# Performance work log

Measured on AMD Instinct MI355X. Metric: run time of the kernel, lower is better.

## Reference

```python
import jax, jax.numpy as jnp
import numpy as np

N_NODES = 50000
N_EDGES = 800000
K_HOPS = 3


def _gcn_norm(edge_index, num_nodes):
    # PyG gcn_norm with add_self_loops=False: sym normalization by target-degree
    row, col = edge_index[0], edge_index[1]  # source j -> target i
    ones = jnp.ones((edge_index.shape[1],), dtype=jnp.float32)
    deg = jax.ops.segment_sum(ones, col, num_segments=num_nodes)
    dinv = jnp.where(deg > 0, 1.0 / jnp.sqrt(deg), 0.0)
    return dinv[row] * dinv[col]  # [E]


def _propagate(h, row, col, norm, num_nodes):
    # out_i = sum_{j->i} norm_e * h_j   (scatter-add over edges)
    msg = h[row] * norm[:, None]  # [E, d]
    return jax.ops.segment_sum(msg, col, num_segments=num_nodes)


def _tag_conv(x, W, b, row, col, norm, num_nodes):
    # out = sum_{k=0..K} (A_norm^k x) @ W[k] + b
    out = x @ W[0]
    h = x
    for k in range(1, K_HOPS + 1):
        h = _propagate(h, row, col, norm, num_nodes)
        out = out + h @ W[k]
    return out + b


def setup_inputs() -> dict:
    key = jax.random.key(0)
    ks = jax.random.split(key, 12)
    x = jax.random.normal(ks[0], (N_NODES, 16), dtype=jnp.float32)
    edge_index = jax.random.randint(ks[1], (2, N_EDGES), 0, N_NODES, dtype=jnp.int64)
    dims = [(16, 64), (64, 64), (64, 64), (64, 64), (64, 4)]
    inp = {"x": x, "edge_index": edge_index}
    for i, (din, dout) in enumerate(dims):
        scale = 1.0 / np.sqrt(din)
        inp[f"W{i}"] = jax.random.normal(ks[2 + 2 * i], (K_HOPS + 1, din, dout), dtype=jnp.float32) * scale
        inp[f"b{i}"] = jnp.zeros((dout,), dtype=jnp.float32)
    return inp


def reference(x, edge_index, W0, b0, W1, b1, W2, b2, W3, b3, W4, b4):
    num_nodes = x.shape[0]
    row, col = edge_index[0], edge_index[1]
    norm = _gcn_norm(edge_index, num_nodes)
    Ws = [W0, W1, W2, W3, W4]
    bs = [b0, b1, b2, b3, b4]
    h = x
    for i in range(4):  # first len(convs)-1 layers: conv -> dropout(identity, eval) -> relu
        h = _tag_conv(h, Ws[i], bs[i], row, col, norm, num_nodes)
        h = jax.nn.relu(h)
    return _tag_conv(h, Ws[4], bs[4], row, col, norm, num_nodes)
```

## Files before the change

### kernel.cpp

```cpp
#include <hip/hip_runtime.h>
#include <hip/hip_fp16.h>

typedef _Float16 f16x8 __attribute__((ext_vector_type(8)));
typedef float f32x4 __attribute__((ext_vector_type(4)));

union H2I { int i; __half2 h; };
static __device__ inline float2 i2f2(int v) {
    H2I u; u.i = v; return __half22float2(u.h);
}
static __device__ inline int f2i2(float a, float b) {
    H2I u; u.h = __floats2half2_rn(a, b); return u.i;
}

struct F8 { float2 a, b, c, d; };
static __device__ inline void fma8(F8& s, int4 g, float w) {
    float2 t;
    t = i2f2(g.x); s.a.x += w * t.x; s.a.y += w * t.y;
    t = i2f2(g.y); s.b.x += w * t.x; s.b.y += w * t.y;
    t = i2f2(g.z); s.c.x += w * t.x; s.c.y += w * t.y;
    t = i2f2(g.w); s.d.x += w * t.x; s.d.y += w * t.y;
}


__global__ __launch_bounds__(256) void count_rank_kernel(const int* __restrict__ col,
                                                         int* __restrict__ cnt,
                                                         int* __restrict__ rank, int E) {
    int e = blockIdx.x * 256 + threadIdx.x;
    if (e < E) rank[e] = atomicAdd(&cnt[col[e]], 1);
}

__global__ __launch_bounds__(256) void scan_block_kernel(const int* __restrict__ cnt,
                                                         int* __restrict__ off,
                                                         int* __restrict__ bsum, int n) {
    const int gid = blockIdx.x * 256 + threadIdx.x;
    const int v = (gid < n) ? cnt[gid] : 0;
    const int lane = threadIdx.x & 63, w = threadIdx.x >> 6;
    int x = v;
#pragma unroll
    for (int d = 1; d < 64; d <<= 1) {
        int t = __shfl_up(x, d);
        if (lane >= d) x += t;
    }
    __shared__ int wt[4];
    if (lane == 63) wt[w] = x;
    __syncthreads();
    int base = 0;
#pragma unroll
    for (int i = 0; i < 3; ++i)
        if (i < w) base += wt[i];
    const int incl = base + x;
    if (gid < n) off[gid] = incl - v;
    if (threadIdx.x == 255) bsum[blockIdx.x] = incl;
}

__global__ __launch_bounds__(256) void scan_bsum_kernel(const int* __restrict__ bsum,
                                                        int* __restrict__ bbase, int nb) {
    const int tid = threadIdx.x;
    const int v = (tid < nb) ? bsum[tid] : 0;
    const int lane = tid & 63, w = tid >> 6;
    int x = v;
#pragma unroll
    for (int d = 1; d < 64; d <<= 1) {
        int t = __shfl_up(x, d);
        if (lane >= d) x += t;
    }
    __shared__ int wt[4];
    if (lane == 63) wt[w] = x;
    __syncthreads();
    int base = 0;
#pragma unroll
    for (int i = 0; i < 3; ++i)
        if (i < w) base += wt[i];
    if (tid < nb) bbase[tid] = base + x - v;
}

__global__ __launch_bounds__(256) void scan_apply_kernel(int* __restrict__ off,
                                                         const int* __restrict__ bbase,
                                                         int n, int E) {
    const int gid = blockIdx.x * 256 + threadIdx.x;
    if (gid < n) off[gid] += bbase[blockIdx.x];
    if (gid == n) off[n] = E;
}

__global__ __launch_bounds__(256) void dinv_kernel(const int* __restrict__ cnt,
                                                   float* __restrict__ dinv, int n) {
    int i = blockIdx.x * 256 + threadIdx.x;
    if (i < n) {
        int c = cnt[i];
        dinv[i] = (c > 0) ? 1.0f / sqrtf((float)c) : 0.0f;
    }
}

__global__ __launch_bounds__(256) void scatter_kernel(const int* __restrict__ row,
                                                      const int* __restrict__ col,
                                                      const int* __restrict__ off,
                                                      const int* __restrict__ rank,
                                                      const float* __restrict__ dinv,
                                                      int2* __restrict__ recs, int E) {
    int e = blockIdx.x * 256 + threadIdx.x;
    if (e >= E) return;
    const int r = row[e], c = col[e];
    const int pos = off[c] + rank[e];
    recs[pos] = make_int2(r, __float_as_int(dinv[r] * dinv[c]));
}

__global__ __launch_bounds__(256) void tohalf_kernel(const float* __restrict__ in,
                                                     __half* __restrict__ xcat, int N) {
    int i = blockIdx.x * 256 + threadIdx.x;
    if (i >= N * 2) return;
    const int n = i >> 1, q = i & 1;
    const float4 v0 = ((const float4*)in)[n * 4 + q * 2 + 0];
    const float4 v1 = ((const float4*)in)[n * 4 + q * 2 + 1];
    int4 o;
    o.x = f2i2(v0.x, v0.y);
    o.y = f2i2(v0.z, v0.w);
    o.z = f2i2(v1.x, v1.y);
    o.w = f2i2(v1.z, v1.w);
    ((int4*)xcat)[n * 8 + q] = o;
}


template <int DQ, int S4>
__global__ __launch_bounds__(256) void gatherh_kernel(const int* __restrict__ off,
                                                      const int2* __restrict__ recs,
                                                      const __half* __restrict__ hin,
                                                      __half* __restrict__ hout, int nNodes) {
    const int t = blockIdx.x * 256 + threadIdx.x;
    const int n = t / DQ;
    const int q = t & (DQ - 1);
    if (n >= nNodes) return;
    const int4* __restrict__ h4 = (const int4*)hin;
    F8 s = {};
    int e = off[n];
    const int e1 = off[n + 1];
    for (; e + 4 <= e1; e += 4) {
        const int2 r0 = recs[e + 0];
        const int2 r1 = recs[e + 1];
        const int2 r2 = recs[e + 2];
        const int2 r3 = recs[e + 3];
        const int4 g0 = h4[r0.x * S4 + q];
        const int4 g1 = h4[r1.x * S4 + q];
        const int4 g2 = h4[r2.x * S4 + q];
        const int4 g3 = h4[r3.x * S4 + q];
        fma8(s, g0, __int_as_float(r0.y));
        fma8(s, g1, __int_as_float(r1.y));
        fma8(s, g2, __int_as_float(r2.y));
        fma8(s, g3, __int_as_float(r3.y));
    }
    for (; e < e1; ++e) {
        const int2 r = recs[e];
        fma8(s, h4[r.x * S4 + q], __int_as_float(r.y));
    }
    int4 o;
    o.x = f2i2(s.a.x, s.a.y);
    o.y = f2i2(s.b.x, s.b.y);
    o.z = f2i2(s.c.x, s.c.y);
    o.w = f2i2(s.d.x, s.d.y);
    ((int4*)hout)[n * S4 + q] = o;
}


__global__ __launch_bounds__(256) void packB_kernel(const float* __restrict__ W,
                                                    __half* __restrict__ Bp, int total) {
    const int t = blockIdx.x * 256 + threadIdx.x;
    if (t >= total) return;
    const int kk = t >> 8;
    const int nt = (t >> 6) & 3;
    const int l = t & 63;
    const int m = l & 15, kg = l >> 4;
    const int col = nt * 16 + m;
    __half tmp[8];
#pragma unroll
    for (int j = 0; j < 8; ++j) {
        const int k = kk * 32 + kg * 8 + j;
        tmp[j] = __float2half(W[k * 64 + col]);
    }
    ((int4*)Bp)[t] = *(int4*)tmp;
}


template <int K>
__global__ __launch_bounds__(256) void gemmcat_mfma(const __half* __restrict__ A,
                                                    const __half* __restrict__ Bp,
                                                    const float* __restrict__ bias,
                                                    __half* __restrict__ out, int N) {
    const int wave = threadIdx.x >> 6;
    const int lane = threadIdx.x & 63;
    const int nb = blockIdx.x * 128 + wave * 32;
    const int m = lane & 15;
    const int kg = lane >> 4;

    const int row0 = min(nb + m, N - 1);
    const int row1 = min(nb + 16 + m, N - 1);
    const f16x8* a0p = (const f16x8*)(A + (size_t)row0 * K + kg * 8);
    const f16x8* a1p = (const f16x8*)(A + (size_t)row1 * K + kg * 8);
    const f16x8* bp = (const f16x8*)Bp + lane;

    f32x4 acc[2][4];
#pragma unroll
    for (int nt = 0; nt < 4; ++nt) {
        const float bv = bias[nt * 16 + m];
        acc[0][nt] = (f32x4){bv, bv, bv, bv};
        acc[1][nt] = (f32x4){bv, bv, bv, bv};
    }

#pragma unroll
    for (int kk = 0; kk < K / 32; ++kk) {
        const f16x8 a0 = a0p[kk * 4];
        const f16x8 a1 = a1p[kk * 4];
#pragma unroll
        for (int nt = 0; nt < 4; ++nt) {
            const f16x8 b = bp[(kk * 4 + nt) * 64];
            acc[0][nt] = __builtin_amdgcn_mfma_f32_16x16x32_f16(a0, b, acc[0][nt], 0, 0, 0);
            acc[1][nt] = __builtin_amdgcn_mfma_f32_16x16x32_f16(a1, b, acc[1][nt], 0, 0, 0);
        }
    }

#pragma unroll
    for (int mt = 0; mt < 2; ++mt) {
#pragma unroll
        for (int nt = 0; nt < 4; ++nt) {
#pragma unroll
            for (int r = 0; r < 4; ++r) {
                const int node = nb + mt * 16 + kg * 4 + r;
                if (node < N) {
                    const float v = fmaxf(acc[mt][nt][r], 0.f);
                    out[(size_t)node * 256 + nt * 16 + m] = __float2half(v);
                }
            }
        }
    }
}


__global__ __launch_bounds__(256) void proj4h_kernel(const __half* __restrict__ h,
                                                     const float* __restrict__ W,
                                                     float* __restrict__ P0,
                                                     float* __restrict__ P1,
                                                     float* __restrict__ P2,
                                                     float* __restrict__ P3, int nNodes) {
    __shared__ float Ws[4 * 64 * 4];
    for (int i = threadIdx.x; i < 1024; i += 256) Ws[i] = W[i];
    __syncthreads();
    const int k = threadIdx.x & 3;
    const int n = blockIdx.x * 64 + (threadIdx.x >> 2);
    if (n >= nNodes) return;
    const int4* __restrict__ h8 = (const int4*)h + (size_t)n * 32;
    const float4* W4 = (const float4*)(Ws + k * 256);
    float4 acc = make_float4(0.f, 0.f, 0.f, 0.f);
#pragma unroll
    for (int i8 = 0; i8 < 8; ++i8) {
        const int4 g = h8[i8];
        const float2 f0 = i2f2(g.x), f1 = i2f2(g.y), f2v = i2f2(g.z), f3 = i2f2(g.w);
        const float hv[8] = {f0.x, f0.y, f1.x, f1.y, f2v.x, f2v.y, f3.x, f3.y};
#pragma unroll
        for (int j = 0; j < 8; ++j) {
            const float4 wr = W4[i8 * 8 + j];
            acc.x += hv[j] * wr.x;
            acc.y += hv[j] * wr.y;
            acc.z += hv[j] * wr.z;
            acc.w += hv[j] * wr.w;
        }
    }
    float4* dst = (k == 0) ? (float4*)P0 : (k == 1) ? (float4*)P1 : (k == 2) ? (float4*)P2
                                                                             : (float4*)P3;
    dst[n] = acc;
}

template <bool FINAL>
__global__ __launch_bounds__(256) void prop1_add_kernel(const int* __restrict__ off,
                                                        const int2* __restrict__ recs,
                                                        const float* __restrict__ Uin,
                                                        const float* __restrict__ P,
                                                        const float* __restrict__ b,
                                                        float* __restrict__ out, int nNodes) {
    const int n = blockIdx.x * 256 + threadIdx.x;
    if (n >= nNodes) return;
    const float4* __restrict__ u4 = (const float4*)Uin;
    float4 acc = ((const float4*)P)[n];
    if (FINAL) {
        const float4 bv = *(const float4*)b;
        acc.x += bv.x;
        acc.y += bv.y;
        acc.z += bv.z;
        acc.w += bv.w;
    }
    int e = off[n];
    const int e1 = off[n + 1];
    for (; e + 4 <= e1; e += 4) {
        const int2 r0 = recs[e + 0];
        const int2 r1 = recs[e + 1];
        const int2 r2 = recs[e + 2];
        const int2 r3 = recs[e + 3];
        const float4 a = u4[r0.x], bb = u4[r1.x], c = u4[r2.x], d = u4[r3.x];
        const float w0 = __int_as_float(r0.y), w1 = __int_as_float(r1.y);
        const float w2 = __int_as_float(r2.y), w3 = __int_as_float(r3.y);
        acc.x += w0 * a.x + w1 * bb.x + w2 * c.x + w3 * d.x;
        acc.y += w0 * a.y + w1 * bb.y + w2 * c.y + w3 * d.y;
        acc.z += w0 * a.z + w1 * bb.z + w2 * c.z + w3 * d.z;
        acc.w += w0 * a.w + w1 * bb.w + w2 * c.w + w3 * d.w;
    }
    for (; e < e1; ++e) {
        const int2 r = recs[e];
        const float ww = __int_as_float(r.y);
        const float4 hv = u4[r.x];
        acc.x += ww * hv.x;
        acc.y += ww * hv.y;
        acc.z += ww * hv.z;
        acc.w += ww * hv.w;
    }
    ((float4*)out)[n] = acc;
}


extern "C" void kernel_launch(void* const* d_in, const int* in_sizes, int n_in,
                              void* d_out, int out_size, void* d_ws, size_t ws_size,
                              hipStream_t stream) {
    const float* x = (const float*)d_in[0];
    const int* ei = (const int*)d_in[1];
    const float* W[5] = {(const float*)d_in[2], (const float*)d_in[4], (const float*)d_in[6],
                         (const float*)d_in[8], (const float*)d_in[10]};
    const float* bb[5] = {(const float*)d_in[3], (const float*)d_in[5], (const float*)d_in[7],
                          (const float*)d_in[9], (const float*)d_in[11]};
    const int E = in_sizes[1] / 2;
    const int N = in_sizes[0] / 16;
    float* outp = (float*)d_out;

    char* p = (char*)d_ws;
    auto alloc = [&](size_t bytes) {
        char* r = p;
        p += (bytes + 255) & ~size_t(255);
        return r;
    };
    const int nb = (N + 255) / 256;
    int* cnt = (int*)alloc((size_t)N * 4);
    int* off = (int*)alloc((size_t)(N + 1) * 4);
    float* dinv = (float*)alloc((size_t)N * 4);
    int* bsum = (int*)alloc((size_t)nb * 4);
    int* bbase = (int*)alloc((size_t)nb * 4);
    int* rank = (int*)alloc((size_t)E * 4);
    int2* recs = (int2*)alloc((size_t)E * 8);
    __half* xcat = (__half*)alloc((size_t)N * 64 * 2);
    __half* hcatA = (__half*)alloc((size_t)N * 256 * 2);
    __half* hcatB = (__half*)alloc((size_t)N * 256 * 2);
    __half* Bp0 = (__half*)alloc((size_t)512 * 8 * 2);
    __half* Bp1 = (__half*)alloc((size_t)2048 * 8 * 2);
    __half* Bp2 = (__half*)alloc((size_t)2048 * 8 * 2);
    __half* Bp3 = (__half*)alloc((size_t)2048 * 8 * 2);
    float* P0 = (float*)alloc((size_t)N * 4 * 4);
    float* P1 = (float*)alloc((size_t)N * 4 * 4);
    float* P2 = (float*)alloc((size_t)N * 4 * 4);
    float* P3 = (float*)alloc((size_t)N * 4 * 4);
    float* Ua = (float*)alloc((size_t)N * 4 * 4);
    float* Ub = (float*)alloc((size_t)N * 4 * 4);

    hipMemsetAsync(cnt, 0, (size_t)N * 4, stream);
    const int eb = (E + 255) / 256;
    count_rank_kernel<<<eb, 256, 0, stream>>>(ei + E, cnt, rank, E);
    scan_block_kernel<<<nb, 256, 0, stream>>>(cnt, off, bsum, N);
    scan_bsum_kernel<<<1, 256, 0, stream>>>(bsum, bbase, nb);
    scan_apply_kernel<<<nb, 256, 0, stream>>>(off, bbase, N, E);
    dinv_kernel<<<nb, 256, 0, stream>>>(cnt, dinv, N);
    scatter_kernel<<<eb, 256, 0, stream>>>(ei, ei + E, off, rank, dinv, recs, E);
    tohalf_kernel<<<(N * 2 + 255) / 256, 256, 0, stream>>>(x, xcat, N);
    packB_kernel<<<2, 256, 0, stream>>>(W[0], Bp0, 512);
    packB_kernel<<<8, 256, 0, stream>>>(W[1], Bp1, 2048);
    packB_kernel<<<8, 256, 0, stream>>>(W[2], Bp2, 2048);
    packB_kernel<<<8, 256, 0, stream>>>(W[3], Bp3, 2048);

    const int gh2 = (N * 2 + 255) / 256;
    const int gh8 = (N * 8 + 255) / 256;
    const int gm = (N + 127) / 128;
    const int gq = (N + 63) / 64;
    const int p1 = (N + 255) / 256;

    gatherh_kernel<2, 8><<<gh2, 256, 0, stream>>>(off, recs, xcat + 0, xcat + 16, N);
    gatherh_kernel<2, 8><<<gh2, 256, 0, stream>>>(off, recs, xcat + 16, xcat + 32, N);
    gatherh_kernel<2, 8><<<gh2, 256, 0, stream>>>(off, recs, xcat + 32, xcat + 48, N);
    gemmcat_mfma<64><<<gm, 256, 0, stream>>>(xcat, Bp0, bb[0], hcatA, N);

    __half* cur = hcatA;
    __half* nxt = hcatB;
    const __half* Bps[4] = {nullptr, Bp1, Bp2, Bp3};
    for (int l = 1; l <= 3; ++l) {
        gatherh_kernel<8, 32><<<gh8, 256, 0, stream>>>(off, recs, cur + 0, cur + 64, N);
        gatherh_kernel<8, 32><<<gh8, 256, 0, stream>>>(off, recs, cur + 64, cur + 128, N);
        gatherh_kernel<8, 32><<<gh8, 256, 0, stream>>>(off, recs, cur + 128, cur + 192, N);
        gemmcat_mfma<256><<<gm, 256, 0, stream>>>(cur, Bps[l], bb[l], nxt, N);
        __half* t = cur;
        cur = nxt;
        nxt = t;
    }

    proj4h_kernel<<<gq, 256, 0, stream>>>(cur, W[4], P0, P1, P2, P3, N);
    prop1_add_kernel<false><<<p1, 256, 0, stream>>>(off, recs, P3, P2, nullptr, Ua, N);
    prop1_add_kernel<false><<<p1, 256, 0, stream>>>(off, recs, Ua, P1, nullptr, Ub, N);
    prop1_add_kernel<true><<<p1, 256, 0, stream>>>(off, recs, Ub, P0, bb[4], outp, N);
}
```

Before: 337.7 us.

## Fuse prep kernels, shrink rank to u16, unroll gather by 8, stage GEMM stores

Merges the dinv, fp16 conversion and four weight-packing launches into one prep kernel to cut launch overhead. Stores per-edge rank as 16-bit to halve that buffer's traffic, which assumes in-degree stays below 65536. Adds an 8-wide unrolled edge loop in the gather to keep more loads in flight. Stages the GEMM output tile in shared memory so each node row is written back with coalesced 16-byte stores, at the cost of extra LDS use and a barrier.

```diff
diff --git a/kernel.cpp b/kernel.cpp
--- a/kernel.cpp
+++ b/kernel.cpp
@@ -24,9 +24,10 @@
 
 __global__ __launch_bounds__(256) void count_rank_kernel(const int* __restrict__ col,
                                                          int* __restrict__ cnt,
-                                                         int* __restrict__ rank, int E) {
+                                                         unsigned short* __restrict__ rank,
+                                                         int E) {
     int e = blockIdx.x * 256 + threadIdx.x;
-    if (e < E) rank[e] = atomicAdd(&cnt[col[e]], 1);
+    if (e < E) rank[e] = (unsigned short)atomicAdd(&cnt[col[e]], 1);
 }
 
 __global__ __launch_bounds__(256) void scan_block_kernel(const int* __restrict__ cnt,
@@ -82,41 +83,76 @@
     if (gid == n) off[n] = E;
 }
 
-__global__ __launch_bounds__(256) void dinv_kernel(const int* __restrict__ cnt,
-                                                   float* __restrict__ dinv, int n) {
-    int i = blockIdx.x * 256 + threadIdx.x;
-    if (i < n) {
-        int c = cnt[i];
-        dinv[i] = (c > 0) ? 1.0f / sqrtf((float)c) : 0.0f;
-    }
+__global__ __launch_bounds__(256) void prep_kernel(const int* __restrict__ cnt,
+                                                   float* __restrict__ dinv,
+                                                   const float* __restrict__ x,
+                                                   __half* __restrict__ xcat,
+                                                   const float* __restrict__ W0,
+                                                   const float* __restrict__ W1,
+                                                   const float* __restrict__ W2,
+                                                   const float* __restrict__ W3,
+                                                   __half* __restrict__ Bp0,
+                                                   __half* __restrict__ Bp1,
+                                                   __half* __restrict__ Bp2,
+                                                   __half* __restrict__ Bp3, int N) {
+    int t = blockIdx.x * 256 + threadIdx.x;
+    if (t < N) {
+        const int c = cnt[t];
+        dinv[t] = (c > 0) ? 1.0f / sqrtf((float)c) : 0.0f;
+        return;
+    }
+    t -= N;
+    if (t < 2 * N) {
+        const int n = t >> 1, q = t & 1;
+        const float4 v0 = ((const float4*)x)[n * 4 + q * 2 + 0];
+        const float4 v1 = ((const float4*)x)[n * 4 + q * 2 + 1];
+        int4 o;
+        o.x = f2i2(v0.x, v0.y);
+        o.y = f2i2(v0.z, v0.w);
+        o.z = f2i2(v1.x, v1.y);
+        o.w = f2i2(v1.z, v1.w);
+        ((int4*)xcat)[n * 8 + q] = o;
+        return;
+    }
+    t -= 2 * N;
+    const float* W;
+    __half* Bp;
+    if (t < 512) {
+        W = W0; Bp = Bp0;
+    } else if (t < 512 + 2048) {
+        W = W1; Bp = Bp1; t -= 512;
+    } else if (t < 512 + 2 * 2048) {
+        W = W2; Bp = Bp2; t -= 512 + 2048;
+    } else if (t < 512 + 3 * 2048) {
+        W = W3; Bp = Bp3; t -= 512 + 2 * 2048;
+    } else {
+        return;
+    }
+    const int kk = t >> 8;
+    const int nt = (t >> 6) & 3;
+    const int l = t & 63;
+    const int m = l & 15, kg = l >> 4;
+    const int col = nt * 16 + m;
+    __half tmp[8];
+#pragma unroll
+    for (int j = 0; j < 8; ++j) {
+        const int k = kk * 32 + kg * 8 + j;
+        tmp[j] = __float2half(W[k * 64 + col]);
+    }
+    ((int4*)Bp)[t] = *(int4*)tmp;
 }
 
 __global__ __launch_bounds__(256) void scatter_kernel(const int* __restrict__ row,
                                                       const int* __restrict__ col,
                                                       const int* __restrict__ off,
-                                                      const int* __restrict__ rank,
+                                                      const unsigned short* __restrict__ rank,
                                                       const float* __restrict__ dinv,
                                                       int2* __restrict__ recs, int E) {
     int e = blockIdx.x * 256 + threadIdx.x;
     if (e >= E) return;
     const int r = row[e], c = col[e];
-    const int pos = off[c] + rank[e];
+    const int pos = off[c] + (int)rank[e];
     recs[pos] = make_int2(r, __float_as_int(dinv[r] * dinv[c]));
-}
-
-__global__ __launch_bounds__(256) void tohalf_kernel(const float* __restrict__ in,
-                                                     __half* __restrict__ xcat, int N) {
-    int i = blockIdx.x * 256 + threadIdx.x;
-    if (i >= N * 2) return;
-    const int n = i >> 1, q = i & 1;
-    const float4 v0 = ((const float4*)in)[n * 4 + q * 2 + 0];
-    const float4 v1 = ((const float4*)in)[n * 4 + q * 2 + 1];
-    int4 o;
-    o.x = f2i2(v0.x, v0.y);
-    o.y = f2i2(v0.z, v0.w);
-    o.z = f2i2(v1.x, v1.y);
-    o.w = f2i2(v1.z, v1.w);
-    ((int4*)xcat)[n * 8 + q] = o;
 }
 
 
@@ -133,6 +169,32 @@
     F8 s = {};
     int e = off[n];
     const int e1 = off[n + 1];
+    for (; e + 8 <= e1; e += 8) {
+        const int2 r0 = recs[e + 0];
+        const int2 r1 = recs[e + 1];
+        const int2 r2 = recs[e + 2];
+        const int2 r3 = recs[e + 3];
+        const int2 r4 = recs[e + 4];
+        const int2 r5 = recs[e + 5];
+        const int2 r6 = recs[e + 6];
+        const int2 r7 = recs[e + 7];
+        const int4 g0 = h4[r0.x * S4 + q];
+        const int4 g1 = h4[r1.x * S4 + q];
+        const int4 g2 = h4[r2.x * S4 + q];
+        const int4 g3 = h4[r3.x * S4 + q];
+        const int4 g4 = h4[r4.x * S4 + q];
+        const int4 g5 = h4[r5.x * S4 + q];
+        const int4 g6 = h4[r6.x * S4 + q];
+        const int4 g7 = h4[r7.x * S4 + q];
+        fma8(s, g0, __int_as_float(r0.y));
+        fma8(s, g1, __int_as_float(r1.y));
+        fma8(s, g2, __int_as_float(r2.y));
+        fma8(s, g3, __int_as_float(r3.y));
+        fma8(s, g4, __int_as_float(r4.y));
+        fma8(s, g5, __int_as_float(r5.y));
+        fma8(s, g6, __int_as_float(r6.y));
+        fma8(s, g7, __int_as_float(r7.y));
+    }
     for (; e + 4 <= e1; e += 4) {
         const int2 r0 = recs[e + 0];
         const int2 r1 = recs[e + 1];
@@ -160,30 +222,12 @@
 }
 
 
-__global__ __launch_bounds__(256) void packB_kernel(const float* __restrict__ W,
-                                                    __half* __restrict__ Bp, int total) {
-    const int t = blockIdx.x * 256 + threadIdx.x;
-    if (t >= total) return;
-    const int kk = t >> 8;
-    const int nt = (t >> 6) & 3;
-    const int l = t & 63;
-    const int m = l & 15, kg = l >> 4;
-    const int col = nt * 16 + m;
-    __half tmp[8];
-#pragma unroll
-    for (int j = 0; j < 8; ++j) {
-        const int k = kk * 32 + kg * 8 + j;
-        tmp[j] = __float2half(W[k * 64 + col]);
-    }
-    ((int4*)Bp)[t] = *(int4*)tmp;
-}
-
-
 template <int K>
 __global__ __launch_bounds__(256) void gemmcat_mfma(const __half* __restrict__ A,
                                                     const __half* __restrict__ Bp,
                                                     const float* __restrict__ bias,
                                                     __half* __restrict__ out, int N) {
+    __shared__ __half hs[128][72];
     const int wave = threadIdx.x >> 6;
     const int lane = threadIdx.x & 63;
     const int nb = blockIdx.x * 128 + wave * 32;
@@ -222,14 +266,22 @@
         for (int nt = 0; nt < 4; ++nt) {
 #pragma unroll
             for (int r = 0; r < 4; ++r) {
-                const int node = nb + mt * 16 + kg * 4 + r;
-                if (node < N) {
-                    const float v = fmaxf(acc[mt][nt][r], 0.f);
-                    out[(size_t)node * 256 + nt * 16 + m] = __float2half(v);
-                }
+                const int nl = wave * 32 + mt * 16 + kg * 4 + r;
+                hs[nl][nt * 16 + m] = __float2half(fmaxf(acc[mt][nt][r], 0.f));
             }
         }
     }
+    __syncthreads();
+    const int nl = threadIdx.x >> 1;
+    const int seg = threadIdx.x & 1;
+    const int node = blockIdx.x * 128 + nl;
+    if (node >= N) return;
+    const int4* src = (const int4*)&hs[nl][seg * 32];
+    int4* dst = (int4*)(out + (size_t)node * 256 + seg * 32);
+    dst[0] = src[0];
+    dst[1] = src[1];
+    dst[2] = src[2];
+    dst[3] = src[3];
 }
 
 
@@ -338,7 +390,7 @@
     float* dinv = (float*)alloc((size_t)N * 4);
     int* bsum = (int*)alloc((size_t)nb * 4);
     int* bbase = (int*)alloc((size_t)nb * 4);
-    int* rank = (int*)alloc((size_t)E * 4);
+    unsigned short* rank = (unsigned short*)alloc((size_t)E * 2);
     int2* recs = (int2*)alloc((size_t)E * 8);
     __half* xcat = (__half*)alloc((size_t)N * 64 * 2);
     __half* hcatA = (__half*)alloc((size_t)N * 256 * 2);
@@ -360,13 +412,10 @@
     scan_block_kernel<<<nb, 256, 0, stream>>>(cnt, off, bsum, N);
     scan_bsum_kernel<<<1, 256, 0, stream>>>(bsum, bbase, nb);
     scan_apply_kernel<<<nb, 256, 0, stream>>>(off, bbase, N, E);
-    dinv_kernel<<<nb, 256, 0, stream>>>(cnt, dinv, N);
+    const int prep_total = 3 * N + 512 + 3 * 2048;
+    prep_kernel<<<(prep_total + 255) / 256, 256, 0, stream>>>(
+        cnt, dinv, x, xcat, W[0], W[1], W[2], W[3], Bp0, Bp1, Bp2, Bp3, N);
     scatter_kernel<<<eb, 256, 0, stream>>>(ei, ei + E, off, rank, dinv, recs, E);
-    tohalf_kernel<<<(N * 2 + 255) / 256, 256, 0, stream>>>(x, xcat, N);
-    packB_kernel<<<2, 256, 0, stream>>>(W[0], Bp0, 512);
-    packB_kernel<<<8, 256, 0, stream>>>(W[1], Bp1, 2048);
-    packB_kernel<<<8, 256, 0, stream>>>(W[2], Bp2, 2048);
-    packB_kernel<<<8, 256, 0, stream>>>(W[3], Bp3, 2048);
 
     const int gh2 = (N * 2 + 255) / 256;
     const int gh8 = (N * 8 + 255) / 256;
```

Measured after the change: 336.5 us. About the same (-0.4%).
